# Optimization experiments

Hardware: AMD Instinct MI355X
Metric: run time of the kernel (lower is better)

## Reference

```python
import jax, jax.numpy as jnp
import numpy as np

N_HEAD = 8
WINDOW = 22   # sliding window size from get_mask()
TRAIN = 29    # per-segment length cap from get_mask()


def _build_mask(T):
    # Banded (sliding-window causal) mask on one segment, tiled 3x3 over segments.
    t = T // 3
    m = np.triu(np.ones((TRAIN, TRAIN), dtype=bool), 1)
    for i in range(WINDOW, TRAIN):
        m[i, : i - WINDOW + 1] = True
    m = np.tile(m[:t, :t], (3, 3))  # [T, T], True = masked out
    return jnp.asarray(m)


def setup_inputs() -> dict:
    key = jax.random.key(0)
    ks = jax.random.split(key, 5)
    B, T, C = 512, 87, 512
    s = 0.02
    return {
        "x": jax.random.normal(ks[0], (B, T, C), dtype=jnp.float32),
        "Wq": jax.random.normal(ks[1], (C, C), dtype=jnp.float32) * s,
        "bq": jnp.zeros((C,), dtype=jnp.float32),
        "Wk": jax.random.normal(ks[2], (C, C), dtype=jnp.float32) * s,
        "bk": jnp.zeros((C,), dtype=jnp.float32),
        "Wv": jax.random.normal(ks[3], (C, C), dtype=jnp.float32) * s,
        "bv": jnp.zeros((C,), dtype=jnp.float32),
        "Wp": jax.random.normal(ks[4], (C, C), dtype=jnp.float32) * s,
        "bp": jnp.zeros((C,), dtype=jnp.float32),
    }


def reference(x, Wq, bq, Wk, bk, Wv, bv, Wp, bp):
    B, T, C = x.shape
    H = N_HEAD
    D = C // H
    # nn.Linear: y = x @ W.T + b
    def split_heads(y):
        return y.reshape(B, T, H, D).transpose(0, 2, 1, 3)  # [B,H,T,D]
    q = split_heads(x @ Wq.T + bq)
    k = split_heads(x @ Wk.T + bk)
    v = split_heads(x @ Wv.T + bv)
    att = jnp.einsum("bhqd,bhkd->bhqk", q, k) * (1.0 / jnp.sqrt(jnp.float32(D)))
    mask = _build_mask(T)  # [T,T] True = disallowed
    att = jnp.where(mask[None, None], -jnp.inf, att)
    att = jax.nn.softmax(att, axis=-1)
    # dropout layers are identity in eval mode
    y = jnp.einsum("bhqk,bhkd->bhqd", att, v)
    y = y.transpose(0, 2, 1, 3).reshape(B, T, C)
    return y @ Wp.T + bp
```

## Files before the change

### kernel.cpp

```cpp
#include <hip/hip_runtime.h>
#include <hip/hip_bf16.h>
#include <stdint.h>

#define B_   512
#define T_   87
#define C_   512
#define H_   8
#define D_   64
#define BT_  44544
#define BH_  4096

typedef __attribute__((ext_vector_type(4))) float f32x4;
typedef __attribute__((ext_vector_type(8))) __bf16 bf16x8;
typedef __attribute__((ext_vector_type(4))) unsigned short u16x4;

__device__ __forceinline__ int mod29(int x) {
  return x < 29 ? x : (x < 58 ? x - 29 : x - 58);
}


__global__ void convert_x_kernel(const float* __restrict__ x,
                                 __hip_bfloat16* __restrict__ xb, int n4) {
  int stride = gridDim.x * blockDim.x;
  for (int i = blockIdx.x * blockDim.x + threadIdx.x; i < n4; i += stride) {
    f32x4 v = ((const f32x4*)x)[i];
    u16x4 o;
    o.x = __builtin_bit_cast(unsigned short, __float2bfloat16(v.x));
    o.y = __builtin_bit_cast(unsigned short, __float2bfloat16(v.y));
    o.z = __builtin_bit_cast(unsigned short, __float2bfloat16(v.z));
    o.w = __builtin_bit_cast(unsigned short, __float2bfloat16(v.w));
    ((u16x4*)xb)[i] = o;
  }
}

__global__ void convert_w_kernel(const float* __restrict__ Wq, const float* __restrict__ Wk,
                                 const float* __restrict__ Wv, const float* __restrict__ Wp,
                                 const float* __restrict__ bq, const float* __restrict__ bk,
                                 const float* __restrict__ bv,
                                 __hip_bfloat16* __restrict__ wqkv,
                                 __hip_bfloat16* __restrict__ wp,
                                 float* __restrict__ biasc) {
  const int NW = 262144;
  const int total = 3 * NW + NW + 1536;
  int stride = gridDim.x * blockDim.x;
  for (int i = blockIdx.x * blockDim.x + threadIdx.x; i < total; i += stride) {
    if (i < 3 * NW) {
      float v = (i < NW) ? Wq[i] : (i < 2 * NW ? Wk[i - NW] : Wv[i - 2 * NW]);
      wqkv[i] = __float2bfloat16(v);
    } else if (i < 4 * NW) {
      wp[i - 3 * NW] = __float2bfloat16(Wp[i - 3 * NW]);
    } else {
      int j = i - 4 * NW;
      biasc[j] = (j < 512) ? bq[j] : (j < 1024 ? bk[j - 512] : bv[j - 1024]);
    }
  }
}


template<int FM, int FN>
__device__ __forceinline__ void compute_tile(const char* Ab, const char* Bb,
                                             int wbM, int wbN, int r16, int r4,
                                             f32x4 acc[FM][FN]) {
  const int cxor = (r16 & 7) << 4;
  bf16x8 bf[FN][2];
#pragma unroll
  for (int fn = 0; fn < FN; ++fn) {
    int row = wbN + fn * 16 + r16;
#pragma unroll
    for (int kk = 0; kk < 2; ++kk)
      bf[fn][kk] = *(const bf16x8*)(Bb + row * 128 + ((kk * 64 + r4 * 16) ^ cxor));
  }
#pragma unroll
  for (int fm = 0; fm < FM; ++fm) {
    int row = wbM + fm * 16 + r16;
    bf16x8 a0 = *(const bf16x8*)(Ab + row * 128 + ((r4 * 16) ^ cxor));
    bf16x8 a1 = *(const bf16x8*)(Ab + row * 128 + ((64 + r4 * 16) ^ cxor));
#pragma unroll
    for (int fn = 0; fn < FN; ++fn) {
      acc[fm][fn] = __builtin_amdgcn_mfma_f32_16x16x32_bf16(a0, bf[fn][0], acc[fm][fn], 0, 0, 0);
      acc[fm][fn] = __builtin_amdgcn_mfma_f32_16x16x32_bf16(a1, bf[fn][1], acc[fm][fn], 0, 0, 0);
    }
  }
}

template<int EPI>
__global__ __launch_bounds__(256) void gemmr_kernel(
    const __hip_bfloat16* __restrict__ A, const __hip_bfloat16* __restrict__ Bt,
    const float* __restrict__ bias, int ntn,
    void* __restrict__ o0, void* __restrict__ o1, void* __restrict__ o2) {
  __shared__ __align__(16) char smem[2][2][16384];

  int tid = threadIdx.x, lane = tid & 63, wave = tid >> 6;
  int r16 = lane & 15, r4 = lane >> 4;

  int nwg = gridDim.x;
  int wg = (blockIdx.x & 7) * (nwg >> 3) + (blockIdx.x >> 3);
  int tileM = (wg / ntn) * 128, tileN = (wg % ntn) * 128;

  int wr = wave >> 1, wc = wave & 1;
  int wbM = wr * 64, wbN = wc * 64;

  const int rbase = tid >> 3, c = tid & 7;
  const int cs = (c ^ (rbase & 7)) << 4;
  const char* Ag = (const char*)A + (size_t)(tileM + rbase) * 1024 + c * 16;
  const char* Bg = (const char*)Bt + (size_t)(tileN + rbase) * 1024 + c * 16;

  f32x4 acc[4][4] = {};
  bf16x8 rA[4], rB[4];

#pragma unroll
  for (int j = 0; j < 4; ++j) {
    rA[j] = *(const bf16x8*)(Ag + (size_t)j * 32768);
    rB[j] = *(const bf16x8*)(Bg + (size_t)j * 32768);
  }
#pragma unroll
  for (int j = 0; j < 4; ++j) {
    *(bf16x8*)(&smem[0][0][0] + (rbase + 32 * j) * 128 + cs) = rA[j];
    *(bf16x8*)(&smem[0][1][0] + (rbase + 32 * j) * 128 + cs) = rB[j];
  }
  __syncthreads();

#pragma unroll
  for (int kt = 0; kt < 8; ++kt) {
    int cur = kt & 1;
    if (kt < 7) {
#pragma unroll
      for (int j = 0; j < 4; ++j) {
        rA[j] = *(const bf16x8*)(Ag + (size_t)j * 32768 + (kt + 1) * 128);
        rB[j] = *(const bf16x8*)(Bg + (size_t)j * 32768 + (kt + 1) * 128);
      }
    }
    __builtin_amdgcn_s_setprio(1);
    compute_tile<4, 4>(&smem[cur][0][0], &smem[cur][1][0], wbM, wbN, r16, r4, acc);
    __builtin_amdgcn_s_setprio(0);
    if (kt < 7) {
#pragma unroll
      for (int j = 0; j < 4; ++j) {
        *(bf16x8*)(&smem[cur ^ 1][0][0] + (rbase + 32 * j) * 128 + cs) = rA[j];
        *(bf16x8*)(&smem[cur ^ 1][1][0] + (rbase + 32 * j) * 128 + cs) = rB[j];
      }
    }
    __syncthreads();
  }

  if constexpr (EPI == 0) {
    char* scratch = &smem[0][0][0] + wave * 2304;
    int gn0 = tileN + wbN;
    int sel = gn0 >> 9;
    int hh = (gn0 & 511) >> 6;
    __hip_bfloat16* obase = (sel == 0) ? (__hip_bfloat16*)o0
                          : (sel == 1) ? (__hip_bfloat16*)o1 : (__hip_bfloat16*)o2;
#pragma unroll
    for (int fm = 0; fm < 4; ++fm) {
#pragma unroll
      for (int fn = 0; fn < 4; ++fn) {
        float bv = bias[gn0 + fn * 16 + r16];
#pragma unroll
        for (int rr = 0; rr < 4; ++rr)
          *(__hip_bfloat16*)(scratch + (r4 * 4 + rr) * 144 + (fn * 16 + r16) * 2) =
              __float2bfloat16(acc[fm][fn][rr] + bv);
      }
#pragma unroll
      for (int p = 0; p < 2; ++p) {
        bf16x8 vrow = *(const bf16x8*)(scratch + (p * 8 + (lane >> 3)) * 144 + (lane & 7) * 16);
        int gm = tileM + wbM + fm * 16 + p * 8 + (lane >> 3);
        int bb = gm / 87, tt = gm - bb * 87;
        *(bf16x8*)(obase + ((size_t)(bb * 8 + hh) * 96 + tt) * 64 + (lane & 7) * 8) = vrow;
      }
    }
  } else {
    char* scratch = &smem[0][0][0] + wave * 4352;
#pragma unroll
    for (int fm = 0; fm < 4; ++fm) {
#pragma unroll
      for (int fn = 0; fn < 4; ++fn) {
        float bv = bias[tileN + wbN + fn * 16 + r16];
#pragma unroll
        for (int rr = 0; rr < 4; ++rr)
          *(float*)(scratch + (r4 * 4 + rr) * 272 + (fn * 16 + r16) * 4) =
              acc[fm][fn][rr] + bv;
      }
#pragma unroll
      for (int p = 0; p < 4; ++p) {
        f32x4 vr = *(const f32x4*)(scratch + (p * 4 + (lane >> 4)) * 272 + (lane & 15) * 16);
        int gm = tileM + wbM + fm * 16 + p * 4 + (lane >> 4);
        *(f32x4*)((float*)o0 + (size_t)gm * 512 + tileN + wbN + (lane & 15) * 4) = vr;
      }
    }
  }
}

#define QS_O  0
#define KS_O  13824
#define VT_O  27648
#define SB_O  40960
#define PB_O  0

__global__ __launch_bounds__(256) void attn_kernel(
    const __hip_bfloat16* __restrict__ q_ws, const __hip_bfloat16* __restrict__ k_ws,
    const __hip_bfloat16* __restrict__ v_ws, __hip_bfloat16* __restrict__ y_ws) {
  __shared__ __align__(16) char smem[77824];
  float* Sb = (float*)(smem + SB_O);

  int tid = threadIdx.x, lane = tid & 63, wave = tid >> 6;
  int bh = blockIdx.x, b = bh >> 3, h = bh & 7;
  int r16 = lane & 15, r4 = lane >> 4;

  {
    const bf16x8* gq = (const bf16x8*)(q_ws + (size_t)bh * 6144);
    const bf16x8* gk = (const bf16x8*)(k_ws + (size_t)bh * 6144);
    const bf16x8* gv = (const bf16x8*)(v_ws + (size_t)bh * 6144);
    for (int i = tid; i < 768; i += 256) {
      int row = i >> 3, ch = i & 7;
      *(bf16x8*)(smem + QS_O + row * 144 + ch * 16) = gq[i];
      *(bf16x8*)(smem + KS_O + row * 144 + ch * 16) = gk[i];
      bf16x8 v8 = gv[i];
      int d0 = ch * 8;
#pragma unroll
      for (int e = 0; e < 8; ++e)
        *(__bf16*)(smem + VT_O + (d0 + e) * 208 + row * 2) = v8[e];
    }
  }
  __syncthreads();

  for (int p = 0; p < 9; ++p) {
    int pair = wave + p * 4;
    int mt = pair / 6, nt = pair - mt * 6;
    f32x4 acc = {0.f, 0.f, 0.f, 0.f};
#pragma unroll
    for (int kk = 0; kk < 2; ++kk) {
      bf16x8 a  = *(const bf16x8*)(smem + QS_O + (mt * 16 + r16) * 144 + kk * 64 + r4 * 16);
      bf16x8 bb = *(const bf16x8*)(smem + KS_O + (nt * 16 + r16) * 144 + kk * 64 + r4 * 16);
      acc = __builtin_amdgcn_mfma_f32_16x16x32_bf16(a, bb, acc, 0, 0, 0);
    }
    int row0 = mt * 16 + r4 * 4, col = nt * 16 + r16;
#pragma unroll
    for (int r = 0; r < 4; ++r) Sb[(row0 + r) * 96 + col] = acc[r];
  }
  __syncthreads();

  int group = tid >> 5, glane = tid & 31;
  for (int r = group; r < 96; r += 8) {
    if (r < 87) {
      int lr = mod29(r);
      float sv[3]; bool al[3];
      float mx = -__builtin_inff();
#pragma unroll
      for (int q = 0; q < 3; ++q) {
        int j = glane + q * 32;
        int lj = mod29(j);
        al[q] = (j < 87) && (lj <= lr) && (lj >= lr - 21);
        sv[q] = al[q] ? Sb[r * 96 + j] * 0.125f : -__builtin_inff();
        mx = fmaxf(mx, sv[q]);
      }
#pragma unroll
      for (int o = 16; o >= 1; o >>= 1) mx = fmaxf(mx, __shfl_xor(mx, o, 32));
      float e[3], sum = 0.f;
#pragma unroll
      for (int q = 0; q < 3; ++q) { e[q] = al[q] ? __expf(sv[q] - mx) : 0.f; sum += e[q]; }
#pragma unroll
      for (int o = 16; o >= 1; o >>= 1) sum += __shfl_xor(sum, o, 32);
      float inv = 1.f / sum;
#pragma unroll
      for (int q = 0; q < 3; ++q)
        *(__hip_bfloat16*)(smem + PB_O + r * 208 + (glane + q * 32) * 2) =
            __float2bfloat16(e[q] * inv);
    } else {
#pragma unroll
      for (int q = 0; q < 3; ++q)
        *(__hip_bfloat16*)(smem + PB_O + r * 208 + (glane + q * 32) * 2) =
            __float2bfloat16(0.f);
    }
  }
  __syncthreads();

  for (int p = 0; p < 6; ++p) {
    int pair = wave + p * 4;
    int mt = pair >> 2, nt = pair & 3;
    f32x4 acc = {0.f, 0.f, 0.f, 0.f};
#pragma unroll
    for (int kk = 0; kk < 3; ++kk) {
      bf16x8 a  = *(const bf16x8*)(smem + PB_O + (mt * 16 + r16) * 208 + kk * 64 + r4 * 16);
      bf16x8 bb = *(const bf16x8*)(smem + VT_O + (nt * 16 + r16) * 208 + kk * 64 + r4 * 16);
      acc = __builtin_amdgcn_mfma_f32_16x16x32_bf16(a, bb, acc, 0, 0, 0);
    }
    int t0 = mt * 16 + r4 * 4, d = nt * 16 + r16;
#pragma unroll
    for (int r = 0; r < 4; ++r) {
      int t = t0 + r;
      if (t < 87)
        y_ws[((size_t)b * 87 + t) * 512 + h * 64 + d] = __float2bfloat16(acc[r]);
    }
  }
}

extern "C" void kernel_launch(void* const* d_in, const int* in_sizes, int n_in,
                              void* d_out, int out_size, void* d_ws, size_t ws_size,
                              hipStream_t stream) {
  const float* x  = (const float*)d_in[0];
  const float* Wq = (const float*)d_in[1];
  const float* bq = (const float*)d_in[2];
  const float* Wk = (const float*)d_in[3];
  const float* bk = (const float*)d_in[4];
  const float* Wv = (const float*)d_in[5];
  const float* bv = (const float*)d_in[6];
  const float* Wp = (const float*)d_in[7];
  const float* bp = (const float*)d_in[8];
  float* out = (float*)d_out;

  char* ws = (char*)d_ws;
  size_t off = 0;
  __hip_bfloat16* xb    = (__hip_bfloat16*)(ws + off); off += (size_t)BT_ * 512 * 2;
  __hip_bfloat16* wqkv  = (__hip_bfloat16*)(ws + off); off += 1536 * 512 * 2;
  __hip_bfloat16* wp    = (__hip_bfloat16*)(ws + off); off += 512 * 512 * 2;
  float*          biasc = (float*)(ws + off);          off += 8192;
  __hip_bfloat16* q_ws  = (__hip_bfloat16*)(ws + off); off += (size_t)BH_ * 6144 * 2;
  __hip_bfloat16* k_ws  = (__hip_bfloat16*)(ws + off); off += (size_t)BH_ * 6144 * 2;
  __hip_bfloat16* v_ws  = (__hip_bfloat16*)(ws + off); off += (size_t)BH_ * 6144 * 2;
  __hip_bfloat16* yb = xb;

  if (ws_size < off) return;

  convert_x_kernel<<<2048, 256, 0, stream>>>(x, xb, BT_ * 512 / 4);
  convert_w_kernel<<<1024, 256, 0, stream>>>(Wq, Wk, Wv, Wp, bq, bk, bv, wqkv, wp, biasc);
  gemmr_kernel<0><<<4176, 256, 0, stream>>>(xb, wqkv, biasc, 12, q_ws, k_ws, v_ws);
  attn_kernel<<<BH_, 256, 0, stream>>>(q_ws, k_ws, v_ws, yb);
  gemmr_kernel<1><<<1392, 256, 0, stream>>>(yb, wp, bp, 4, out, nullptr, nullptr);
}
```

Measured before the change: 268.8 us.

## Fuse QK^T and softmax in registers, swizzle transposed V in LDS

The attention kernel now keeps each wave's 16x96 score tile in MFMA accumulators and applies the mask and softmax there, using shuffles across the 16 column lanes. This removes the fp32 score staging buffer in LDS and one barrier, and shrinks LDS use, which may let more blocks fit per CU. The transposed V store gets an XOR swizzle on 16-byte chunks to cut bank conflicts on the scattered writes and the PV reads. With 6 row tiles across 4 waves, two waves do double work, so load is uneven across waves.

```diff
diff --git a/kernel.cpp b/kernel.cpp
--- a/kernel.cpp
+++ b/kernel.cpp
@@ -193,14 +193,12 @@
 #define QS_O  0
 #define KS_O  13824
 #define VT_O  27648
-#define SB_O  40960
-#define PB_O  0
+#define PB_O  40960
 
 __global__ __launch_bounds__(256) void attn_kernel(
     const __hip_bfloat16* __restrict__ q_ws, const __hip_bfloat16* __restrict__ k_ws,
     const __hip_bfloat16* __restrict__ v_ws, __hip_bfloat16* __restrict__ y_ws) {
-  __shared__ __align__(16) char smem[77824];
-  float* Sb = (float*)(smem + SB_O);
+  __shared__ __align__(16) char smem[60928];
 
   int tid = threadIdx.x, lane = tid & 63, wave = tid >> 6;
   int bh = blockIdx.x, b = bh >> 3, h = bh & 7;
@@ -215,61 +213,68 @@
       *(bf16x8*)(smem + QS_O + row * 144 + ch * 16) = gq[i];
       *(bf16x8*)(smem + KS_O + row * 144 + ch * 16) = gk[i];
       bf16x8 v8 = gv[i];
-      int d0 = ch * 8;
-#pragma unroll
-      for (int e = 0; e < 8; ++e)
-        *(__bf16*)(smem + VT_O + (d0 + e) * 208 + row * 2) = v8[e];
+      int tc = row >> 3, tb = (row & 7) << 1, xr = ch & 3;
+#pragma unroll
+      for (int e = 0; e < 8; ++e) {
+        int d = ch * 8 + e;
+        *(__bf16*)(smem + VT_O + d * 208 + ((tc ^ xr) << 4) + tb) = v8[e];
+      }
     }
   }
   __syncthreads();
 
-  for (int p = 0; p < 9; ++p) {
-    int pair = wave + p * 4;
-    int mt = pair / 6, nt = pair - mt * 6;
-    f32x4 acc = {0.f, 0.f, 0.f, 0.f};
+  int ljv[6]; bool cok[6];
+#pragma unroll
+  for (int j = 0; j < 6; ++j) {
+    int col = j * 16 + r16;
+    ljv[j] = mod29(col);
+    cok[j] = col < 87;
+  }
+
+  for (int m = wave; m < 6; m += 4) {
+    f32x4 s[6] = {};
 #pragma unroll
     for (int kk = 0; kk < 2; ++kk) {
-      bf16x8 a  = *(const bf16x8*)(smem + QS_O + (mt * 16 + r16) * 144 + kk * 64 + r4 * 16);
-      bf16x8 bb = *(const bf16x8*)(smem + KS_O + (nt * 16 + r16) * 144 + kk * 64 + r4 * 16);
-      acc = __builtin_amdgcn_mfma_f32_16x16x32_bf16(a, bb, acc, 0, 0, 0);
-    }
-    int row0 = mt * 16 + r4 * 4, col = nt * 16 + r16;
-#pragma unroll
-    for (int r = 0; r < 4; ++r) Sb[(row0 + r) * 96 + col] = acc[r];
-  }
-  __syncthreads();
-
-  int group = tid >> 5, glane = tid & 31;
-  for (int r = group; r < 96; r += 8) {
-    if (r < 87) {
-      int lr = mod29(r);
-      float sv[3]; bool al[3];
-      float mx = -__builtin_inff();
-#pragma unroll
-      for (int q = 0; q < 3; ++q) {
-        int j = glane + q * 32;
-        int lj = mod29(j);
-        al[q] = (j < 87) && (lj <= lr) && (lj >= lr - 21);
-        sv[q] = al[q] ? Sb[r * 96 + j] * 0.125f : -__builtin_inff();
-        mx = fmaxf(mx, sv[q]);
-      }
-#pragma unroll
-      for (int o = 16; o >= 1; o >>= 1) mx = fmaxf(mx, __shfl_xor(mx, o, 32));
-      float e[3], sum = 0.f;
-#pragma unroll
-      for (int q = 0; q < 3; ++q) { e[q] = al[q] ? __expf(sv[q] - mx) : 0.f; sum += e[q]; }
-#pragma unroll
-      for (int o = 16; o >= 1; o >>= 1) sum += __shfl_xor(sum, o, 32);
-      float inv = 1.f / sum;
-#pragma unroll
-      for (int q = 0; q < 3; ++q)
-        *(__hip_bfloat16*)(smem + PB_O + r * 208 + (glane + q * 32) * 2) =
-            __float2bfloat16(e[q] * inv);
-    } else {
-#pragma unroll
-      for (int q = 0; q < 3; ++q)
-        *(__hip_bfloat16*)(smem + PB_O + r * 208 + (glane + q * 32) * 2) =
-            __float2bfloat16(0.f);
+      bf16x8 aq = *(const bf16x8*)(smem + QS_O + (m * 16 + r16) * 144 + kk * 64 + r4 * 16);
+#pragma unroll
+      for (int j = 0; j < 6; ++j) {
+        bf16x8 kb = *(const bf16x8*)(smem + KS_O + (j * 16 + r16) * 144 + kk * 64 + r4 * 16);
+        s[j] = __builtin_amdgcn_mfma_f32_16x16x32_bf16(aq, kb, s[j], 0, 0, 0);
+      }
+    }
+#pragma unroll
+    for (int rr = 0; rr < 4; ++rr) {
+      int row = m * 16 + r4 * 4 + rr;
+      bool rok = row < 87;
+      int lr = mod29(row);
+      float mxv = -1e30f;
+#pragma unroll
+      for (int j = 0; j < 6; ++j) {
+        bool al = rok && cok[j] && (ljv[j] <= lr) && (ljv[j] + 21 >= lr);
+        float sv = al ? s[j][rr] * 0.125f : -1e30f;
+        s[j][rr] = sv;
+        mxv = fmaxf(mxv, sv);
+      }
+      mxv = fmaxf(mxv, __shfl_xor(mxv, 1));
+      mxv = fmaxf(mxv, __shfl_xor(mxv, 2));
+      mxv = fmaxf(mxv, __shfl_xor(mxv, 4));
+      mxv = fmaxf(mxv, __shfl_xor(mxv, 8));
+      float sm = 0.f;
+#pragma unroll
+      for (int j = 0; j < 6; ++j) {
+        float e = __expf(s[j][rr] - mxv);
+        s[j][rr] = e;
+        sm += e;
+      }
+      sm += __shfl_xor(sm, 1);
+      sm += __shfl_xor(sm, 2);
+      sm += __shfl_xor(sm, 4);
+      sm += __shfl_xor(sm, 8);
+      float inv = rok ? 1.f / sm : 0.f;
+#pragma unroll
+      for (int j = 0; j < 6; ++j)
+        *(__hip_bfloat16*)(smem + PB_O + row * 208 + (j * 16 + r16) * 2) =
+            __float2bfloat16(s[j][rr] * inv);
     }
   }
   __syncthreads();
@@ -277,14 +282,16 @@
   for (int p = 0; p < 6; ++p) {
     int pair = wave + p * 4;
     int mt = pair >> 2, nt = pair & 3;
+    int d = nt * 16 + r16;
+    int dx = (d >> 3) & 3;
     f32x4 acc = {0.f, 0.f, 0.f, 0.f};
 #pragma unroll
     for (int kk = 0; kk < 3; ++kk) {
       bf16x8 a  = *(const bf16x8*)(smem + PB_O + (mt * 16 + r16) * 208 + kk * 64 + r4 * 16);
-      bf16x8 bb = *(const bf16x8*)(smem + VT_O + (nt * 16 + r16) * 208 + kk * 64 + r4 * 16);
+      bf16x8 bb = *(const bf16x8*)(smem + VT_O + d * 208 + (((kk * 4 + r4) ^ dx) << 4));
       acc = __builtin_amdgcn_mfma_f32_16x16x32_bf16(a, bb, acc, 0, 0, 0);
     }
-    int t0 = mt * 16 + r4 * 4, d = nt * 16 + r16;
+    int t0 = mt * 16 + r4 * 4;
 #pragma unroll
     for (int r = 0; r < 4; ++r) {
       int t = t0 + r;
```

After: 237.7 us. 1.13x faster.
